# Optimization experiments

Measured on AMD Instinct MI355X. Metric: run time of the kernel, lower is better.

The kernel has to match this reference:

```python
import jax, jax.numpy as jnp
import numpy as np

B, S, D_IN, D, H = 2, 2048, 512, 1024, 16
HD = D // H


def _linear_params(key, d_in, d_out):
    kw, kb = jax.random.split(key)
    bound = 1.0 / np.sqrt(d_in)
    W = jax.random.uniform(kw, (d_in, d_out), jnp.float32, -bound, bound)
    b = jax.random.uniform(kb, (d_out,), jnp.float32, -bound, bound)
    return W, b


def setup_inputs() -> dict:
    key = jax.random.key(0)
    keys = jax.random.split(key, 8)
    x = jax.random.normal(keys[0], (B, S, D_IN), jnp.float32)
    We, be = _linear_params(keys[1], D_IN, D)
    Wq, bq = _linear_params(keys[2], D, D)
    Wk, bk = _linear_params(keys[3], D, D)
    Wv, bv = _linear_params(keys[4], D, D)
    W0, b0 = _linear_params(keys[5], D, D)
    W1, b1 = _linear_params(keys[6], D, D)
    W2, b2 = _linear_params(keys[7], D, D)
    return {"x": x, "We": We, "be": be, "Wq": Wq, "bq": bq, "Wk": Wk, "bk": bk,
            "Wv": Wv, "bv": bv, "W0": W0, "b0": b0, "W1": W1, "b1": b1, "W2": W2, "b2": b2}


def reference(x, We, be, Wq, bq, Wk, bk, Wv, bv, W0, b0, W1, b1, W2, b2):
    # embedding
    e = x @ We + be                                   # [B,S,D]
    q = (e @ Wq + bq).reshape(B, S, H, HD)            # [B,S,H,hd]
    k = (e @ Wk + bk).reshape(B, S, H, HD)
    v = (e @ Wv + bv).reshape(B, S, H, HD)
    scale = 1.0 / jnp.sqrt(jnp.float32(HD))
    scores = jnp.einsum('bqhd,bkhd->bhqk', q, k) * scale
    attn = jax.nn.softmax(scores, axis=-1)            # [B,H,S,S]
    ctx = jnp.einsum('bhqk,bkhd->bqhd', attn, v).reshape(B, S, D)
    mha = e + (ctx @ W0 + b0)                         # residual
    ffn = jax.nn.relu(mha @ W1 + b1) @ W2 + b2
    return mha + ffn
```

## Files before the change

### kernel.cpp

```cpp
#include <hip/hip_runtime.h>

typedef unsigned short u16;
typedef __bf16 bf16x8 __attribute__((ext_vector_type(8)));
typedef float f32x4 __attribute__((ext_vector_type(4)));

__device__ __forceinline__ float bf2f(u16 u) {
  return __builtin_bit_cast(float, (unsigned)u << 16);
}
__device__ __forceinline__ u16 f2bf(float f) {
  unsigned u = __builtin_bit_cast(unsigned, f);
  u += 0x7FFFu + ((u >> 16) & 1u);
  return (u16)(u >> 16);
}
__device__ __forceinline__ unsigned pk2(float a, float b) {
  return (unsigned)f2bf(a) | ((unsigned)f2bf(b) << 16);
}
__device__ __forceinline__ unsigned pk2t(float a, float b) {
  return __builtin_amdgcn_perm(__builtin_bit_cast(unsigned, b),
                               __builtin_bit_cast(unsigned, a), 0x07060302u);
}
__device__ __forceinline__ f32x4 mfma16(bf16x8 a, bf16x8 b, f32x4 c) {
  return __builtin_amdgcn_mfma_f32_16x16x32_bf16(a, b, c, 0, 0, 0);
}
__device__ __forceinline__ void async_cp16(const u16* g, u16* l) {
  __builtin_amdgcn_global_load_lds((const __attribute__((address_space(1))) void*)g,
                                   (__attribute__((address_space(3))) void*)l, 16, 0, 0);
}
#define S_BARRIER() asm volatile("s_barrier" ::: "memory")

__global__ __launch_bounds__(256) void cast_f32_bf16(const float* __restrict__ in,
                                                     u16* __restrict__ out, int n) {
  int idx = (blockIdx.x * 256 + threadIdx.x) * 4;
  if (idx < n) {
    float4 f = *(const float4*)&in[idx];
    ushort4 o;
    o.x = f2bf(f.x); o.y = f2bf(f.y); o.z = f2bf(f.z); o.w = f2bf(f.w);
    *(ushort4*)&out[idx] = o;
  }
}

__global__ __launch_bounds__(256) void biascat(const float* __restrict__ bq,
                                               const float* __restrict__ bk,
                                               const float* __restrict__ bv,
                                               float* __restrict__ o) {
  int i = blockIdx.x * 256 + threadIdx.x;
  if (i < 3072)
    o[i] = i < 1024 ? bq[i] : (i < 2048 ? bk[i - 1024] : bv[i - 2048]);
}

#define TSP 72
__global__ __launch_bounds__(256) void transpose_weights(
    const float* __restrict__ We, const float* __restrict__ Wq,
    const float* __restrict__ Wk, const float* __restrict__ Wv,
    const float* __restrict__ W0, const float* __restrict__ W1,
    const float* __restrict__ W2, u16* Wet, u16* qkvWt, u16* W0t, u16* W1t,
    u16* W2t) {
  const int z = blockIdx.z;
  const float* in;
  u16* out;
  int out_rs = 1024;
  if (z == 0) { if (blockIdx.y >= 8) return; in = We; out = Wet; out_rs = 512; }
  else if (z == 1) { in = Wq; out = qkvWt; }
  else if (z == 2) { in = Wk; out = qkvWt + 1048576; }
  else if (z == 3) { in = Wv; out = qkvWt + 2097152; }
  else if (z == 4) { in = W0; out = W0t; }
  else if (z == 5) { in = W1; out = W1t; }
  else { in = W2; out = W2t; }
  __shared__ alignas(16) u16 T[64][TSP];
  const int tid = threadIdx.x;
  const int r0 = blockIdx.y * 64, c0 = blockIdx.x * 64;
#pragma unroll
  for (int it = 0; it < 4; ++it) {
    int vi = it * 256 + tid;
    int i = vi >> 4, j4 = (vi & 15) * 4;
    float4 f = *(const float4*)&in[(size_t)(r0 + i) * 1024 + c0 + j4];
    T[i][j4 + 0] = f2bf(f.x);
    T[i][j4 + 1] = f2bf(f.y);
    T[i][j4 + 2] = f2bf(f.z);
    T[i][j4 + 3] = f2bf(f.w);
  }
  __syncthreads();
#pragma unroll
  for (int it = 0; it < 2; ++it) {
    int vi = it * 256 + tid;
    int i = vi >> 3, j8 = (vi & 7) * 8;
    bf16x8 v;
#pragma unroll
    for (int u = 0; u < 8; ++u) ((u16*)&v)[u] = T[j8 + u][i];
    *(bf16x8*)&out[(size_t)(c0 + i) * out_rs + r0 + j8] = v;
  }
}

template <int TM>
__global__ __launch_bounds__(256, (TM == 128) ? 3 : 5) void gemm_mfma(
    const u16* __restrict__ A, const u16* __restrict__ Bt,
    const float* __restrict__ bias, const u16* __restrict__ res,
    void* __restrict__ Cout, int M, int N, int K, int relu, int f32out) {
  constexpr int MT = TM / 32;
  constexpr int AI = TM / 32;
  __shared__ alignas(16) u16 As[2][TM * 64];
  __shared__ alignas(16) u16 Bs[2][64 * 64];
  const int tid = threadIdx.x;
  const int wave = tid >> 6, lane = tid & 63;
  const int quad = lane >> 4, l16 = lane & 15;
  const int ib = blockIdx.x;
  int by, bx;
  if constexpr (TM == 128) { by = (ib & 7) * 4 + ((ib >> 3) & 3); bx = ib >> 5; }
  else { by = (ib & 7) * 8 + ((ib >> 3) & 7); bx = ib >> 6; }
  const int m0 = by * TM, n0 = bx * 64;
  const int wm = (wave & 1) * (TM / 2), wn = (wave >> 1) * 32;

  f32x4 acc[MT][2];
#pragma unroll
  for (int i = 0; i < MT; ++i)
#pragma unroll
    for (int j = 0; j < 2; ++j) acc[i][j] = (f32x4){0.f, 0.f, 0.f, 0.f};

  const int srow = lane >> 3;
  const int schunk = (lane & 7) ^ (srow & 7);
  const u16* Ag = A + (size_t)(m0 + wave * (TM / 4) + srow) * K + schunk * 8;
  const u16* Bg = Bt + (size_t)(n0 + wave * 16 + srow) * K + schunk * 8;
  u16* AsW0 = &As[0][wave * (TM / 4) * 64];
  u16* BsW0 = &Bs[0][wave * 16 * 64];
  u16* AsW1 = &As[1][wave * (TM / 4) * 64];
  u16* BsW1 = &Bs[1][wave * 16 * 64];

#define GEMM_ISSUE(ab, bb, k)                                     \
  {                                                               \
    _Pragma("unroll") for (int i = 0; i < AI; ++i)                \
        async_cp16(Ag + (k) + (size_t)i * 8 * K, (ab) + i * 512); \
    _Pragma("unroll") for (int i = 0; i < 2; ++i)                 \
        async_cp16(Bg + (k) + (size_t)i * 8 * K, (bb) + i * 512); \
  }

  GEMM_ISSUE(AsW0, BsW0, 0);
  const int T = K >> 6;
  const int swz = (l16 & 7);
  for (int t = 0; t < T; ++t) {
    const int cb = t & 1;
    S_BARRIER();
    const int kn = (t + 1 < T) ? ((t + 1) << 6) : 0;
    if (cb == 0) GEMM_ISSUE(AsW1, BsW1, kn) else GEMM_ISSUE(AsW0, BsW0, kn);
    if constexpr (TM == 128)
      asm volatile("s_waitcnt vmcnt(6)" ::: "memory");
    else
      asm volatile("s_waitcnt vmcnt(4)" ::: "memory");
    S_BARRIER();
#pragma unroll
    for (int kk = 0; kk < 2; ++kk) {
      bf16x8 af[MT], bfr[2];
#pragma unroll
      for (int mt = 0; mt < MT; ++mt)
        af[mt] = *(const bf16x8*)&As[cb][(wm + mt * 16 + l16) * 64 +
                                        ((kk * 4 + quad) ^ swz) * 8];
#pragma unroll
      for (int nt = 0; nt < 2; ++nt)
        bfr[nt] = *(const bf16x8*)&Bs[cb][(wn + nt * 16 + l16) * 64 +
                                          ((kk * 4 + quad) ^ swz) * 8];
#pragma unroll
      for (int mt = 0; mt < MT; ++mt)
#pragma unroll
        for (int nt = 0; nt < 2; ++nt)
          acc[mt][nt] = mfma16(af[mt], bfr[nt], acc[mt][nt]);
    }
  }
  asm volatile("s_waitcnt vmcnt(0)" ::: "memory");

#pragma unroll
  for (int nt = 0; nt < 2; ++nt) {
    int col = n0 + wn + nt * 16 + l16;
    float bv = bias[col];
#pragma unroll
    for (int mt = 0; mt < MT; ++mt) {
#pragma unroll
      for (int r = 0; r < 4; ++r) {
        int row = m0 + wm + mt * 16 + quad * 4 + r;
        float v = acc[mt][nt][r] + bv;
        if (res) v += bf2f(res[(size_t)row * N + col]);
        if (relu) v = fmaxf(v, 0.f);
        if (f32out)
          ((float*)Cout)[(size_t)row * N + col] = v;
        else
          ((u16*)Cout)[(size_t)row * N + col] = f2bf(v);
      }
    }
  }
}

__global__ __launch_bounds__(256, 2) void attn_kernel(
    const u16* __restrict__ QKV, const u16* __restrict__ Vt,
    u16* __restrict__ O) {
  __shared__ alignas(16) u16 Ks[2][64 * 64];
  __shared__ alignas(16) u16 Vs[2][64 * 64];
  __shared__ alignas(16) u16 Ps[4][32 * 64];
  const int tid = threadIdx.x;
  const int wave = tid >> 6, lane = tid & 63;
  const int quad = lane >> 4, l16 = lane & 15;
  const int ib = blockIdx.x;
  const int bh = ib & 31, b = bh >> 4, h = bh & 15;
  const int q0 = (ib >> 5) * 128 + wave * 32;

  bf16x8 qf[2][2];
#pragma unroll
  for (int qt = 0; qt < 2; ++qt) {
    const size_t qoff = (size_t)(b * 2048 + q0 + qt * 16 + l16) * 3072 + h * 64;
#pragma unroll
    for (int kk = 0; kk < 2; ++kk) {
      bf16x8 raw = *(const bf16x8*)&QKV[qoff + kk * 32 + quad * 8];
#pragma unroll
      for (int u = 0; u < 8; ++u)
        ((u16*)&raw)[u] = f2bf(0.125f * bf2f(((u16*)&raw)[u]));
      qf[qt][kk] = raw;
    }
  }
  bf16x8 ones;
#pragma unroll
  for (int u = 0; u < 8; ++u) ((u16*)&ones)[u] = 0x3F80;

  f32x4 o[4][2];
  f32x4 l_acc[2] = {(f32x4){0.f, 0.f, 0.f, 0.f}, (f32x4){0.f, 0.f, 0.f, 0.f}};
#pragma unroll
  for (int mt = 0; mt < 4; ++mt)
#pragma unroll
    for (int qt = 0; qt < 2; ++qt) o[mt][qt] = (f32x4){0.f, 0.f, 0.f, 0.f};

  const int srow = lane >> 3;
  const int schunk = (lane & 7) ^ (srow & 7);
  const u16* Kg = QKV + (size_t)(b * 2048 + wave * 16 + srow) * 3072 + 1024 +
                  h * 64 + schunk * 8;
  const u16* Vg = Vt + (size_t)((b * 16 + h) * 64 + wave * 16 + srow) * 2048 +
                  schunk * 8;
  u16* KsW0 = &Ks[0][(wave * 16) * 64];
  u16* VsW0 = &Vs[0][(wave * 16) * 64];
  u16* KsW1 = &Ks[1][(wave * 16) * 64];
  u16* VsW1 = &Vs[1][(wave * 16) * 64];

#define ATTN_ISSUE(kb, vb, kt)                                \
  {                                                           \
    async_cp16(Kg + (size_t)(kt) * 3072, (kb));               \
    async_cp16(Kg + (size_t)((kt) + 8) * 3072, (kb) + 512);   \
    async_cp16(Vg + (kt), (vb));                              \
    async_cp16(Vg + (kt) + (size_t)8 * 2048, (vb) + 512);     \
  }

  ATTN_ISSUE(KsW0, VsW0, 0);
  const int swz = (l16 & 7);
  u16* PsW = &Ps[wave][0];
  for (int t = 0; t < 32; ++t) {
    const int cb = t & 1;
    S_BARRIER();
    const int ktn = (t + 1 < 32) ? ((t + 1) * 64) : 0;
    if (cb == 0) ATTN_ISSUE(KsW1, VsW1, ktn) else ATTN_ISSUE(KsW0, VsW0, ktn);
    asm volatile("s_waitcnt vmcnt(4)" ::: "memory");
    S_BARRIER();

    f32x4 st[4][2];
#pragma unroll
    for (int km = 0; km < 4; ++km)
#pragma unroll
      for (int qt = 0; qt < 2; ++qt) st[km][qt] = (f32x4){0.f, 0.f, 0.f, 0.f};
    __builtin_amdgcn_s_setprio(1);
#pragma unroll
    for (int kk = 0; kk < 2; ++kk)
#pragma unroll
      for (int km = 0; km < 4; ++km) {
        bf16x8 kf = *(const bf16x8*)&Ks[cb][(km * 16 + l16) * 64 +
                                           ((kk * 4 + quad) ^ swz) * 8];
        st[km][0] = mfma16(kf, qf[0][kk], st[km][0]);
        st[km][1] = mfma16(kf, qf[1][kk], st[km][1]);
      }
    __builtin_amdgcn_s_setprio(0);

#pragma unroll
    for (int qt = 0; qt < 2; ++qt)
#pragma unroll
      for (int km = 0; km < 4; ++km) {
        float e0 = __expf(st[km][qt][0]), e1 = __expf(st[km][qt][1]);
        float e2 = __expf(st[km][qt][2]), e3 = __expf(st[km][qt][3]);
        uint2 pk;
        pk.x = pk2t(e0, e1);
        pk.y = pk2t(e2, e3);
        *(uint2*)&PsW[(qt * 16 + l16) * 64 +
                      ((km * 2 + (quad >> 1)) ^ swz) * 8 + (quad & 1) * 4] = pk;
      }
    asm volatile("s_waitcnt lgkmcnt(0)" ::: "memory");

    __builtin_amdgcn_s_setprio(1);
#pragma unroll
    for (int kk2 = 0; kk2 < 2; ++kk2) {
      bf16x8 pf0 =
          *(const bf16x8*)&PsW[l16 * 64 + ((kk2 * 4 + quad) ^ swz) * 8];
      bf16x8 pf1 = *(const bf16x8*)&PsW[(16 + l16) * 64 +
                                        ((kk2 * 4 + quad) ^ swz) * 8];
      l_acc[0] = mfma16(ones, pf0, l_acc[0]);
      l_acc[1] = mfma16(ones, pf1, l_acc[1]);
#pragma unroll
      for (int mt = 0; mt < 4; ++mt) {
        bf16x8 vf = *(const bf16x8*)&Vs[cb][(mt * 16 + l16) * 64 +
                                           ((kk2 * 4 + quad) ^ swz) * 8];
        o[mt][0] = mfma16(vf, pf0, o[mt][0]);
        o[mt][1] = mfma16(vf, pf1, o[mt][1]);
      }
    }
    __builtin_amdgcn_s_setprio(0);
  }
  asm volatile("s_waitcnt vmcnt(0)" ::: "memory");

#pragma unroll
  for (int qt = 0; qt < 2; ++qt) {
    float inv = 1.f / l_acc[qt][0];
    size_t base = (size_t)(b * 2048 + q0 + qt * 16 + l16) * 1024 + h * 64;
#pragma unroll
    for (int mt = 0; mt < 4; ++mt) {
      uint2 pk;
      pk.x = pk2(o[mt][qt][0] * inv, o[mt][qt][1] * inv);
      pk.y = pk2(o[mt][qt][2] * inv, o[mt][qt][3] * inv);
      *(uint2*)&O[base + mt * 16 + quad * 4] = pk;
    }
  }
}

__global__ __launch_bounds__(256) void transpose_v(const u16* __restrict__ QKV,
                                                   u16* __restrict__ vt) {
  const int bh = blockIdx.y;
  const int b = bh >> 4, h = bh & 15;
  const int s0 = blockIdx.x * 64;
  const u16* in = QKV + (size_t)b * 2048 * 3072 + 2048 + h * 64;
  u16* out = vt + (size_t)bh * 131072;
  __shared__ alignas(16) u16 T[64][TSP];
  const int tid = threadIdx.x;
#pragma unroll
  for (int it = 0; it < 2; ++it) {
    int vi = it * 256 + tid;
    int i = vi >> 3, j8 = (vi & 7) * 8;
    *(bf16x8*)&T[i][j8] = *(const bf16x8*)&in[(size_t)(s0 + i) * 3072 + j8];
  }
  __syncthreads();
#pragma unroll
  for (int it = 0; it < 2; ++it) {
    int vi = it * 256 + tid;
    int i = vi >> 3, j8 = (vi & 7) * 8;
    bf16x8 vv;
#pragma unroll
    for (int u = 0; u < 8; ++u) ((u16*)&vv)[u] = T[j8 + u][i];
    *(bf16x8*)&out[(size_t)i * 2048 + s0 + j8] = vv;
  }
}

extern "C" void kernel_launch(void* const* d_in, const int* in_sizes, int n_in,
                              void* d_out, int out_size, void* d_ws,
                              size_t ws_size, hipStream_t stream) {
  const float* x = (const float*)d_in[0];
  const float* We = (const float*)d_in[1];
  const float* be = (const float*)d_in[2];
  const float* Wq = (const float*)d_in[3];
  const float* bq = (const float*)d_in[4];
  const float* Wk = (const float*)d_in[5];
  const float* bk = (const float*)d_in[6];
  const float* Wv = (const float*)d_in[7];
  const float* bv = (const float*)d_in[8];
  const float* W0 = (const float*)d_in[9];
  const float* b0 = (const float*)d_in[10];
  const float* W1 = (const float*)d_in[11];
  const float* b1 = (const float*)d_in[12];
  const float* W2 = (const float*)d_in[13];
  const float* b2 = (const float*)d_in[14];

  u16* ws = (u16*)d_ws;
  u16* xb = ws;
  u16* Wet = xb + 2097152;
  u16* qkvWt = Wet + 524288;
  u16* ctx = ws;
  u16* W0t = qkvWt + 3145728;
  u16* W1t = W0t + 1048576;
  u16* W2t = W1t + 1048576;
  float* biasqkv = (float*)(W2t + 1048576);
  u16* e = W2t + 1048576 + 6144;
  u16* qkv = e + 4194304;
  u16* vtb = qkv + 12582912;
  u16* mha = qkv;
  u16* h1 = e;

  cast_f32_bf16<<<2048, 256, 0, stream>>>(x, xb, 4096 * 512);
  transpose_weights<<<dim3(16, 16, 7), 256, 0, stream>>>(
      We, Wq, Wk, Wv, W0, W1, W2, Wet, qkvWt, W0t, W1t, W2t);
  biascat<<<12, 256, 0, stream>>>(bq, bk, bv, biasqkv);

  gemm_mfma<128><<<512, 256, 0, stream>>>(xb, Wet, be, nullptr, e, 4096, 1024,
                                          512, 0, 0);
  gemm_mfma<128><<<1536, 256, 0, stream>>>(e, qkvWt, biasqkv, nullptr, qkv,
                                           4096, 3072, 1024, 0, 0);
  transpose_v<<<dim3(32, 32), 256, 0, stream>>>(qkv, vtb);
  attn_kernel<<<512, 256, 0, stream>>>(qkv, vtb, ctx);
  gemm_mfma<128><<<512, 256, 0, stream>>>(ctx, W0t, b0, e, mha, 4096, 1024,
                                          1024, 0, 0);
  gemm_mfma<128><<<512, 256, 0, stream>>>(mha, W1t, b1, nullptr, h1, 4096,
                                          1024, 1024, 1, 0);
  gemm_mfma<128><<<512, 256, 0, stream>>>(h1, W2t, b2, mha, d_out, 4096, 1024,
                                          1024, 0, 1);
}
```

Measured before the change: 268.5 us.

## Fuse prep kernels, double attention KV tile, shrink GEMM tiles for occupancy

Merges the input cast, weight transposes and QKV bias concatenation into one prep launch, which removes two kernel launches. The attention kernel now stages 128 keys per iteration instead of 64, with a new swizzled V load pattern, which halves the number of barrier and prefetch rounds. The four N=1024 GEMMs switch to a 64-wide tile template with twice as many blocks, to fill more compute units. Larger LDS tiles may reduce attention occupancy, and smaller GEMM tiles lower data reuse.

```diff
diff --git a/kernel.cpp b/kernel.cpp
--- a/kernel.cpp
+++ b/kernel.cpp
@@ -28,34 +28,32 @@
 }
 #define S_BARRIER() asm volatile("s_barrier" ::: "memory")
 
-__global__ __launch_bounds__(256) void cast_f32_bf16(const float* __restrict__ in,
-                                                     u16* __restrict__ out, int n) {
-  int idx = (blockIdx.x * 256 + threadIdx.x) * 4;
-  if (idx < n) {
-    float4 f = *(const float4*)&in[idx];
-    ushort4 o;
-    o.x = f2bf(f.x); o.y = f2bf(f.y); o.z = f2bf(f.z); o.w = f2bf(f.w);
-    *(ushort4*)&out[idx] = o;
-  }
-}
-
-__global__ __launch_bounds__(256) void biascat(const float* __restrict__ bq,
-                                               const float* __restrict__ bk,
-                                               const float* __restrict__ bv,
-                                               float* __restrict__ o) {
-  int i = blockIdx.x * 256 + threadIdx.x;
-  if (i < 3072)
-    o[i] = i < 1024 ? bq[i] : (i < 2048 ? bk[i - 1024] : bv[i - 2048]);
-}
-
 #define TSP 72
-__global__ __launch_bounds__(256) void transpose_weights(
+__global__ __launch_bounds__(256) void prep_fused(
     const float* __restrict__ We, const float* __restrict__ Wq,
     const float* __restrict__ Wk, const float* __restrict__ Wv,
     const float* __restrict__ W0, const float* __restrict__ W1,
-    const float* __restrict__ W2, u16* Wet, u16* qkvWt, u16* W0t, u16* W1t,
-    u16* W2t) {
+    const float* __restrict__ W2, const float* __restrict__ x,
+    const float* __restrict__ bq, const float* __restrict__ bk,
+    const float* __restrict__ bv, u16* Wet, u16* qkvWt, u16* W0t, u16* W1t,
+    u16* W2t, u16* xb, float* biasqkv) {
   const int z = blockIdx.z;
+  const int tid = threadIdx.x;
+  if (z >= 7) {
+    if (z == 15) {
+      int i = (blockIdx.y * 16 + blockIdx.x) * 256 + tid;
+      if (i < 3072)
+        biasqkv[i] = i < 1024 ? bq[i] : (i < 2048 ? bk[i - 1024] : bv[i - 2048]);
+      return;
+    }
+    int blin = (z - 7) * 256 + blockIdx.y * 16 + blockIdx.x;
+    int idx = (blin * 256 + tid) * 4;
+    float4 f = *(const float4*)&x[idx];
+    ushort4 o;
+    o.x = f2bf(f.x); o.y = f2bf(f.y); o.z = f2bf(f.z); o.w = f2bf(f.w);
+    *(ushort4*)&xb[idx] = o;
+    return;
+  }
   const float* in;
   u16* out;
   int out_rs = 1024;
@@ -67,7 +65,6 @@
   else if (z == 5) { in = W1; out = W1t; }
   else { in = W2; out = W2t; }
   __shared__ alignas(16) u16 T[64][TSP];
-  const int tid = threadIdx.x;
   const int r0 = blockIdx.y * 64, c0 = blockIdx.x * 64;
 #pragma unroll
   for (int it = 0; it < 4; ++it) {
@@ -190,8 +187,8 @@
 __global__ __launch_bounds__(256, 2) void attn_kernel(
     const u16* __restrict__ QKV, const u16* __restrict__ Vt,
     u16* __restrict__ O) {
-  __shared__ alignas(16) u16 Ks[2][64 * 64];
-  __shared__ alignas(16) u16 Vs[2][64 * 64];
+  __shared__ alignas(16) u16 Ks[2][128 * 64];
+  __shared__ alignas(16) u16 Vs[2][64 * 128];
   __shared__ alignas(16) u16 Ps[4][32 * 64];
   const int tid = threadIdx.x;
   const int wave = tid >> 6, lane = tid & 63;
@@ -226,83 +223,90 @@
 
   const int srow = lane >> 3;
   const int schunk = (lane & 7) ^ (srow & 7);
-  const u16* Kg = QKV + (size_t)(b * 2048 + wave * 16 + srow) * 3072 + 1024 +
+  const u16* Kg = QKV + (size_t)(b * 2048 + wave * 32 + srow) * 3072 + 1024 +
                   h * 64 + schunk * 8;
-  const u16* Vg = Vt + (size_t)((b * 16 + h) * 64 + wave * 16 + srow) * 2048 +
-                  schunk * 8;
-  u16* KsW0 = &Ks[0][(wave * 16) * 64];
-  u16* VsW0 = &Vs[0][(wave * 16) * 64];
-  u16* KsW1 = &Ks[1][(wave * 16) * 64];
-  u16* VsW1 = &Vs[1][(wave * 16) * 64];
-
-#define ATTN_ISSUE(kb, vb, kt)                                \
-  {                                                           \
-    async_cp16(Kg + (size_t)(kt) * 3072, (kb));               \
-    async_cp16(Kg + (size_t)((kt) + 8) * 3072, (kb) + 512);   \
-    async_cp16(Vg + (kt), (vb));                              \
-    async_cp16(Vg + (kt) + (size_t)8 * 2048, (vb) + 512);     \
-  }
-
-  ATTN_ISSUE(KsW0, VsW0, 0);
+  const int vr = lane >> 4, vc = lane & 15;
+  const u16* Vg = Vt + (size_t)((b * 16 + h) * 64 + wave * 16 + vr) * 2048;
+  u16* KsW0 = &Ks[0][wave * 32 * 64];
+  u16* KsW1 = &Ks[1][wave * 32 * 64];
+  u16* VsW0 = &Vs[0][wave * 16 * 128];
+  u16* VsW1 = &Vs[1][wave * 16 * 128];
+
+#define ATTN_ISSUE2(kb, vb, kt)                                              \
+  {                                                                          \
+    _Pragma("unroll") for (int i = 0; i < 4; ++i)                            \
+        async_cp16(Kg + (size_t)((kt) + i * 8) * 3072, (kb) + i * 512);      \
+    _Pragma("unroll") for (int i = 0; i < 4; ++i)                            \
+        async_cp16(Vg + (size_t)(i * 4) * 2048 + (kt) +                      \
+                       (vc ^ ((i * 4 + vr) & 7)) * 8,                        \
+                   (vb) + i * 512);                                          \
+  }
+
+  ATTN_ISSUE2(KsW0, VsW0, 0);
   const int swz = (l16 & 7);
   u16* PsW = &Ps[wave][0];
-  for (int t = 0; t < 32; ++t) {
+  for (int t = 0; t < 16; ++t) {
     const int cb = t & 1;
     S_BARRIER();
-    const int ktn = (t + 1 < 32) ? ((t + 1) * 64) : 0;
-    if (cb == 0) ATTN_ISSUE(KsW1, VsW1, ktn) else ATTN_ISSUE(KsW0, VsW0, ktn);
-    asm volatile("s_waitcnt vmcnt(4)" ::: "memory");
+    const int ktn = (t + 1 < 16) ? ((t + 1) * 128) : 0;
+    if (cb == 0) ATTN_ISSUE2(KsW1, VsW1, ktn) else ATTN_ISSUE2(KsW0, VsW0, ktn);
+    asm volatile("s_waitcnt vmcnt(8)" ::: "memory");
     S_BARRIER();
 
-    f32x4 st[4][2];
-#pragma unroll
-    for (int km = 0; km < 4; ++km)
-#pragma unroll
-      for (int qt = 0; qt < 2; ++qt) st[km][qt] = (f32x4){0.f, 0.f, 0.f, 0.f};
-    __builtin_amdgcn_s_setprio(1);
-#pragma unroll
-    for (int kk = 0; kk < 2; ++kk)
-#pragma unroll
-      for (int km = 0; km < 4; ++km) {
-        bf16x8 kf = *(const bf16x8*)&Ks[cb][(km * 16 + l16) * 64 +
-                                           ((kk * 4 + quad) ^ swz) * 8];
-        st[km][0] = mfma16(kf, qf[0][kk], st[km][0]);
-        st[km][1] = mfma16(kf, qf[1][kk], st[km][1]);
+#pragma unroll
+    for (int sub = 0; sub < 2; ++sub) {
+      f32x4 st[4][2];
+#pragma unroll
+      for (int km = 0; km < 4; ++km)
+#pragma unroll
+        for (int qt = 0; qt < 2; ++qt) st[km][qt] = (f32x4){0.f, 0.f, 0.f, 0.f};
+      __builtin_amdgcn_s_setprio(1);
+#pragma unroll
+      for (int kk = 0; kk < 2; ++kk)
+#pragma unroll
+        for (int km = 0; km < 4; ++km) {
+          bf16x8 kf = *(const bf16x8*)&Ks[cb][(sub * 64 + km * 16 + l16) * 64 +
+                                             ((kk * 4 + quad) ^ swz) * 8];
+          st[km][0] = mfma16(kf, qf[0][kk], st[km][0]);
+          st[km][1] = mfma16(kf, qf[1][kk], st[km][1]);
+        }
+      __builtin_amdgcn_s_setprio(0);
+
+#pragma unroll
+      for (int qt = 0; qt < 2; ++qt)
+#pragma unroll
+        for (int km = 0; km < 4; ++km) {
+          float e0 = __expf(st[km][qt][0]), e1 = __expf(st[km][qt][1]);
+          float e2 = __expf(st[km][qt][2]), e3 = __expf(st[km][qt][3]);
+          uint2 pk;
+          pk.x = pk2t(e0, e1);
+          pk.y = pk2t(e2, e3);
+          *(uint2*)&PsW[(qt * 16 + l16) * 64 +
+                        ((km * 2 + (quad >> 1)) ^ swz) * 8 + (quad & 1) * 4] =
+              pk;
+        }
+      asm volatile("s_waitcnt lgkmcnt(0)" ::: "memory");
+
+      __builtin_amdgcn_s_setprio(1);
+#pragma unroll
+      for (int kk2 = 0; kk2 < 2; ++kk2) {
+        bf16x8 pf0 =
+            *(const bf16x8*)&PsW[l16 * 64 + ((kk2 * 4 + quad) ^ swz) * 8];
+        bf16x8 pf1 = *(const bf16x8*)&PsW[(16 + l16) * 64 +
+                                          ((kk2 * 4 + quad) ^ swz) * 8];
+        l_acc[0] = mfma16(ones, pf0, l_acc[0]);
+        l_acc[1] = mfma16(ones, pf1, l_acc[1]);
+#pragma unroll
+        for (int mt = 0; mt < 4; ++mt) {
+          bf16x8 vf = *(const bf16x8*)&Vs[cb][(mt * 16 + l16) * 128 +
+                                             (sub * 8 +
+                                              ((kk2 * 4 + quad) ^ swz)) * 8];
+          o[mt][0] = mfma16(vf, pf0, o[mt][0]);
+          o[mt][1] = mfma16(vf, pf1, o[mt][1]);
+        }
       }
-    __builtin_amdgcn_s_setprio(0);
-
-#pragma unroll
-    for (int qt = 0; qt < 2; ++qt)
-#pragma unroll
-      for (int km = 0; km < 4; ++km) {
-        float e0 = __expf(st[km][qt][0]), e1 = __expf(st[km][qt][1]);
-        float e2 = __expf(st[km][qt][2]), e3 = __expf(st[km][qt][3]);
-        uint2 pk;
-        pk.x = pk2t(e0, e1);
-        pk.y = pk2t(e2, e3);
-        *(uint2*)&PsW[(qt * 16 + l16) * 64 +
-                      ((km * 2 + (quad >> 1)) ^ swz) * 8 + (quad & 1) * 4] = pk;
-      }
-    asm volatile("s_waitcnt lgkmcnt(0)" ::: "memory");
-
-    __builtin_amdgcn_s_setprio(1);
-#pragma unroll
-    for (int kk2 = 0; kk2 < 2; ++kk2) {
-      bf16x8 pf0 =
-          *(const bf16x8*)&PsW[l16 * 64 + ((kk2 * 4 + quad) ^ swz) * 8];
-      bf16x8 pf1 = *(const bf16x8*)&PsW[(16 + l16) * 64 +
-                                        ((kk2 * 4 + quad) ^ swz) * 8];
-      l_acc[0] = mfma16(ones, pf0, l_acc[0]);
-      l_acc[1] = mfma16(ones, pf1, l_acc[1]);
-#pragma unroll
-      for (int mt = 0; mt < 4; ++mt) {
-        bf16x8 vf = *(const bf16x8*)&Vs[cb][(mt * 16 + l16) * 64 +
-                                           ((kk2 * 4 + quad) ^ swz) * 8];
-        o[mt][0] = mfma16(vf, pf0, o[mt][0]);
-        o[mt][1] = mfma16(vf, pf1, o[mt][1]);
-      }
-    }
-    __builtin_amdgcn_s_setprio(0);
+      __builtin_amdgcn_s_setprio(0);
+    }
   }
   asm volatile("s_waitcnt vmcnt(0)" ::: "memory");
 
@@ -381,21 +385,20 @@
   u16* mha = qkv;
   u16* h1 = e;
 
-  cast_f32_bf16<<<2048, 256, 0, stream>>>(x, xb, 4096 * 512);
-  transpose_weights<<<dim3(16, 16, 7), 256, 0, stream>>>(
-      We, Wq, Wk, Wv, W0, W1, W2, Wet, qkvWt, W0t, W1t, W2t);
-  biascat<<<12, 256, 0, stream>>>(bq, bk, bv, biasqkv);
-
-  gemm_mfma<128><<<512, 256, 0, stream>>>(xb, Wet, be, nullptr, e, 4096, 1024,
+  prep_fused<<<dim3(16, 16, 16), 256, 0, stream>>>(
+      We, Wq, Wk, Wv, W0, W1, W2, x, bq, bk, bv, Wet, qkvWt, W0t, W1t, W2t,
+      xb, biasqkv);
+
+  gemm_mfma<64><<<1024, 256, 0, stream>>>(xb, Wet, be, nullptr, e, 4096, 1024,
                                           512, 0, 0);
   gemm_mfma<128><<<1536, 256, 0, stream>>>(e, qkvWt, biasqkv, nullptr, qkv,
                                            4096, 3072, 1024, 0, 0);
   transpose_v<<<dim3(32, 32), 256, 0, stream>>>(qkv, vtb);
   attn_kernel<<<512, 256, 0, stream>>>(qkv, vtb, ctx);
-  gemm_mfma<128><<<512, 256, 0, stream>>>(ctx, W0t, b0, e, mha, 4096, 1024,
+  gemm_mfma<64><<<1024, 256, 0, stream>>>(ctx, W0t, b0, e, mha, 4096, 1024,
                                           1024, 0, 0);
-  gemm_mfma<128><<<512, 256, 0, stream>>>(mha, W1t, b1, nullptr, h1, 4096,
+  gemm_mfma<64><<<1024, 256, 0, stream>>>(mha, W1t, b1, nullptr, h1, 4096,
                                           1024, 1024, 1, 0);
-  gemm_mfma<128><<<512, 256, 0, stream>>>(h1, W2t, b2, mha, d_out, 4096, 1024,
+  gemm_mfma<64><<<1024, 256, 0, stream>>>(h1, W2t, b2, mha, d_out, 4096, 1024,
                                           1024, 0, 1);
 }
```

Result: faster. 249.8 us (-7.0%).
